# Performance work log

Hardware: AMD Instinct MI355X
Metric: run time of the kernel (lower is better)

## Reference

```python
import jax, jax.numpy as jnp
import numpy as np


def _resize_axis(x, axis, out_size):
    # PyTorch bilinear interpolate, align_corners=False, no antialias (half-pixel centers)
    in_size = x.shape[axis]
    src = (jnp.arange(out_size) + 0.5) * (in_size / out_size) - 0.5
    src = jnp.clip(src, 0.0, in_size - 1.0)
    lo = jnp.floor(src).astype(jnp.int32)
    hi = jnp.minimum(lo + 1, in_size - 1)
    w = (src - lo).astype(x.dtype)
    shp = [1] * x.ndim
    shp[axis] = out_size
    w = w.reshape(shp)
    return jnp.take(x, lo, axis=axis) * (1 - w) + jnp.take(x, hi, axis=axis) * w


def _bilinear(x, h, w):
    return _resize_axis(_resize_axis(x, 2, h), 3, w)


def _unfold3(x):
    # F.unfold(kernel_size=3, padding=1) -> [B, C, 9, H*W], kernel offsets row-major
    B, C, H, W = x.shape
    xp = jnp.pad(x, ((0, 0), (0, 0), (1, 1), (1, 1)))
    pats = jnp.stack([xp[:, :, dy:dy + H, dx:dx + W] for dy in range(3) for dx in range(3)], axis=2)
    return pats.reshape(B, C, 9, H * W)


def setup_inputs() -> dict:
    key = jax.random.key(0)
    ks = jax.random.split(key, 7)
    B, C, H, W = 4, 64, 192, 192
    return {
        "x": jax.random.normal(ks[0], (B, C, H, W), jnp.float32),
        "gn_weight": jnp.ones((C,), jnp.float32) + 0.1 * jax.random.normal(ks[1], (C,), jnp.float32),
        "gn_bias": 0.1 * jax.random.normal(ks[2], (C,), jnp.float32),
        "w1": jax.random.normal(ks[3], (2 * C, C), jnp.float32) / np.sqrt(C).astype(np.float32),
        "b1": 0.01 * jax.random.normal(ks[4], (2 * C,), jnp.float32),
        "w2": jax.random.normal(ks[5], (C, 2 * C), jnp.float32) / np.sqrt(2 * C).astype(np.float32),
        "b2": 0.01 * jax.random.normal(ks[6], (C,), jnp.float32),
    }


def reference(x, gn_weight, gn_bias, w1, b1, w2, b2):
    B, C, H, W = x.shape
    MIN_CONN, MAX_CONN, THRESHOLD, POWER = 1, 16, 0.3, 2
    KSQ = 9
    K_MAX = min(MAX_CONN, KSQ)
    EPS_NORM = 1e-12

    x_down = _bilinear(x, H // 2, W // 2)
    x_du = _bilinear(x_down, H, W)
    df = jnp.abs(x - x_du).sum(1, keepdims=True)            # [B,1,H,W]
    dmin = df.reshape(B, -1).min(1).reshape(B, 1, 1, 1)
    dmax = df.reshape(B, -1).max(1).reshape(B, 1, 1, 1)
    dfp = ((df - dmin) / (dmax - dmin + 1e-8)) ** POWER
    mask = (dfp > THRESHOLD).astype(x.dtype)
    conn = MIN_CONN + jnp.clip(jnp.round(dfp * (MAX_CONN - MIN_CONN)), 0) * mask
    counts = conn.reshape(B, H * W)                          # [B,HW]
    process = counts > 1

    # ---- per-pixel cosine similarity to 3x3 neighborhood ----
    patches = _unfold3(x)                                    # [B,C,9,HW]
    x_flat = x.reshape(B, C, H * W)
    xn = x_flat / jnp.maximum(jnp.linalg.norm(x_flat, axis=1, keepdims=True), EPS_NORM)
    pn = patches / jnp.maximum(jnp.linalg.norm(patches, axis=1, keepdims=True), EPS_NORM)
    sim = jnp.einsum('bcn,bckn->bkn', xn, pn)                # [B,9,HW]

    # ---- adaptive top-k (k = min(count, 9)) + exp-softmax weighted sum of raw patches ----
    order = jnp.argsort(-sim, axis=1)                        # descending over the 9 neighbors
    sim_s = jnp.take_along_axis(sim, order, axis=1)
    pat_s = jnp.take_along_axis(patches, jnp.broadcast_to(order[:, None], patches.shape), axis=2)
    k = jnp.minimum(counts, K_MAX)                           # [B,HW]
    keep = (jnp.arange(KSQ)[None, :, None] < k[:, None, :]).astype(x.dtype)
    wts = jnp.exp(sim_s) * keep
    wts = wts / jnp.maximum(wts.sum(1, keepdims=True), EPS_NORM)
    weighted = jnp.einsum('bckn,bkn->bcn', pat_s, wts)       # [B,C,HW]
    output = jnp.where(process[:, None, :], weighted, x_flat).reshape(B, C, H, W)

    # ---- GroupNorm(32, C) on identity ----
    G = 32
    xg = x.reshape(B, G, C // G, H, W)
    mu = xg.mean((2, 3, 4), keepdims=True)
    var = xg.var((2, 3, 4), keepdims=True)
    nx = ((xg - mu) / jnp.sqrt(var + 1e-5)).reshape(B, C, H, W)
    norm_x = nx * gn_weight[None, :, None, None] + gn_bias[None, :, None, None]

    enhanced = output + norm_x
    # ---- conv_ffn: 1x1 conv C->2C, ReLU, 1x1 conv 2C->C ----
    h1 = jax.nn.relu(jnp.einsum('oc,bchw->bohw', w1, enhanced) + b1[None, :, None, None])
    ffn = jnp.einsum('oc,bchw->bohw', w2, h1) + b2[None, :, None, None]
    return enhanced + ffn
```

## Files before the change

kernel.cpp:

```cpp
#include <hip/hip_runtime.h>
#include <hip/hip_bf16.h>

#define BB 4
#define CC 64
#define HH 192
#define WW 192
#define HWSZ (HH*WW)
#define HD 96
#define WD 96
#define GG 32
#define FTH 512
#define FPX 128
#define FBPB (HWSZ/FPX)
#define PBLK 128
#define BPB (HWSZ/PBLK)

typedef short short8 __attribute__((ext_vector_type(8)));
typedef float f32x4  __attribute__((ext_vector_type(4)));

__device__ __forceinline__ unsigned short f2bf(float f) {
    unsigned u = __float_as_uint(f);
    return (unsigned short)((u + 0x7FFFu + ((u >> 16) & 1u)) >> 16);
}
__device__ __forceinline__ float bf2f(unsigned short s) {
    return __uint_as_float(((unsigned)s) << 16);
}
__device__ __forceinline__ unsigned pk2(float a, float b) {
    return (unsigned)f2bf(a) | ((unsigned)f2bf(b) << 16);
}
__device__ __forceinline__ short8 u4s8(uint4 u) {
    union { uint4 a; short8 b; } cvt; cvt.a = u; return cvt.b;
}

__device__ __forceinline__ int swz1152(int bid) {
    return (bid & 7) * 144 + (bid >> 3);
}

__global__ __launch_bounds__(256) void k_pre(const float* __restrict__ x,
                                             const float* __restrict__ w1,
                                             const float* __restrict__ w2,
                                             unsigned* __restrict__ wf,
                                             float* __restrict__ df,
                                             float* __restrict__ nrm,
                                             float* __restrict__ gnacc,
                                             unsigned* __restrict__ mmmin,
                                             unsigned* __restrict__ mmmax) {
    __shared__ float sgn[64];
    __shared__ float wmn[4], wmx[4];
    int tid = threadIdx.x;
    if (tid < 64) sgn[tid] = 0.f;
    __syncthreads();

    if (blockIdx.x < 16) {
        #pragma unroll
        for (int rep = 0; rep < 2; ++rep) {
            int i = blockIdx.x*512 + rep*256 + tid;
            if (i < 4096) {
                float2 v = ((const float2*)w1)[i];
                int j = i >> 5, cp = i & 31, c0 = cp << 1;
                int fi = ((j >> 4) << 1) + (c0 >> 5);
                int ln = (((c0 & 31) >> 3) << 4) + (j & 15);
                wf[fi*256 + ln*4 + (cp & 3)] = pk2(v.x, v.y);
            } else {
                int i2 = i - 4096;
                float2 v = ((const float2*)w2)[i2];
                int c = i2 >> 6, jp = i2 & 63, j0 = jp << 1;
                int fi = ((j0 >> 5) << 2) + (c >> 4);
                int ln = (((j0 & 31) >> 3) << 4) + (c & 15);
                wf[4096 + fi*256 + ln*4 + (jp & 3)] = pk2(v.x, v.y);
            }
        }
    }

    int virt = swz1152(blockIdx.x);
    int b = virt / BPB;
    int pb = (virt % BPB) * PBLK;
    int wave = tid >> 6, lane = tid & 63;
    int oct = lane >> 3, grp = lane & 7;
    int p0 = pb + wave*32 + grp*4;
    int h = p0 / WW, w0 = p0 % WW;

    float hs = fminf(fmaxf(0.5f*(float)h - 0.25f, 0.f), 95.f);
    int hl = (int)hs; int hh2 = min(hl+1, 95); float fh = hs - (float)hl;
    int r0 = 2*hl, r1 = 2*hh2;

    int t0 = min(max(w0/2 - 1, 0), 92);
    float wc[4][4];
    #pragma unroll
    for (int i = 0; i < 4; ++i) {
        float wsr = fminf(fmaxf(0.5f*(float)(w0+i) - 0.25f, 0.f), 95.f);
        int wl = (int)wsr; int wh = min(wl+1, 95); float fw = wsr - (float)wl;
        int kl = wl - t0, kh = wh - t0;
        #pragma unroll
        for (int k = 0; k < 4; ++k)
            wc[i][k] = ((k==kl) ? (1.f-fw) : 0.f) + ((k==kh) ? fw : 0.f);
    }

    const float* xb = x + (size_t)b*CC*HWSZ;
    float d[4]  = {0.f,0.f,0.f,0.f};
    float qn[4] = {0.f,0.f,0.f,0.f};
    float gs[4] = {0.f,0.f,0.f,0.f};
    float gq[4] = {0.f,0.f,0.f,0.f};
    #pragma unroll
    for (int cc = 0; cc < 8; ++cc) {
        const float* pc = xb + (size_t)(oct*8 + cc)*HWSZ;
        float4 xc = *(const float4*)(pc + h*WW + w0);
        const float* pa = pc + r0*WW + 2*t0;
        const float* pq = pc + r1*WW + 2*t0;
        float T[4];
        #pragma unroll
        for (int k = 0; k < 4; ++k) {
            float2 a0 = *(const float2*)(pa + 2*k);
            float2 a1 = *(const float2*)(pa + WW + 2*k);
            float2 c0 = *(const float2*)(pq + 2*k);
            float2 c1 = *(const float2*)(pq + WW + 2*k);
            float xdA = 0.25f*((a0.x + a1.x) + (a0.y + a1.y));
            float xdB = 0.25f*((c0.x + c1.x) + (c0.y + c1.y));
            T[k] = (1.f-fh)*xdA + fh*xdB;
        }
        float xv[4] = {xc.x, xc.y, xc.z, xc.w};
        float sch = 0.f, qch = 0.f;
        #pragma unroll
        for (int i = 0; i < 4; ++i) {
            float du = (wc[i][0]*T[0] + wc[i][1]*T[1]) + (wc[i][2]*T[2] + wc[i][3]*T[3]);
            d[i] += fabsf(xv[i] - du);
            float x2 = xv[i]*xv[i];
            qn[i] += x2;
            sch += xv[i];
            qch += x2;
        }
        gs[cc>>1] += sch;
        gq[cc>>1] += qch;
    }
    #pragma unroll
    for (int o = 8; o <= 32; o <<= 1) {
        #pragma unroll
        for (int i = 0; i < 4; ++i) {
            d[i]  += __shfl_xor(d[i], o);
            qn[i] += __shfl_xor(qn[i], o);
        }
    }
    if (oct == 0) {
        *(float4*)(df  + (size_t)b*HWSZ + p0) = make_float4(d[0], d[1], d[2], d[3]);
        *(float4*)(nrm + (size_t)b*HWSZ + p0) =
            make_float4(sqrtf(qn[0]), sqrtf(qn[1]), sqrtf(qn[2]), sqrtf(qn[3]));
    }
    float mn = fminf(fminf(d[0], d[1]), fminf(d[2], d[3]));
    float mx = fmaxf(fmaxf(d[0], d[1]), fmaxf(d[2], d[3]));
    #pragma unroll
    for (int o = 1; o < 64; o <<= 1) {
        mn = fminf(mn, __shfl_xor(mn, o));
        mx = fmaxf(mx, __shfl_xor(mx, o));
    }
    if (lane == 0) { wmn[wave] = mn; wmx[wave] = mx; }
    #pragma unroll
    for (int o = 1; o <= 4; o <<= 1) {
        #pragma unroll
        for (int j = 0; j < 4; ++j) {
            gs[j] += __shfl_xor(gs[j], o);
            gq[j] += __shfl_xor(gq[j], o);
        }
    }
    if (grp == 0) {
        #pragma unroll
        for (int j = 0; j < 4; ++j) {
            atomicAdd(&sgn[2*(oct*4+j)],   gs[j]);
            atomicAdd(&sgn[2*(oct*4+j)+1], gq[j]);
        }
    }
    __syncthreads();
    if (tid < 64) atomicAdd(&gnacc[(size_t)b*64 + tid], sgn[tid]);
    if (tid == 0) {
        float bmn = fminf(fminf(wmn[0], wmn[1]), fminf(wmn[2], wmn[3]));
        float bmx = fmaxf(fmaxf(wmx[0], wmx[1]), fmaxf(wmx[2], wmx[3]));
        atomicMin(&mmmin[b], __float_as_uint(bmn));
        atomicMax(&mmmax[b], __float_as_uint(bmx));
    }
}

__global__ __launch_bounds__(FTH, 4) void k_fused(const float* __restrict__ x,
                                                  const float* __restrict__ df,
                                                  const float* __restrict__ nrm,
                                                  const unsigned* __restrict__ mmmin,
                                                  const unsigned* __restrict__ mmmax,
                                                  const float* __restrict__ gnacc,
                                                  const float* __restrict__ gw,
                                                  const float* __restrict__ gb,
                                                  const unsigned* __restrict__ wf,
                                                  const float* __restrict__ b1,
                                                  const float* __restrict__ b2,
                                                  float* __restrict__ out) {
    __shared__ __align__(16) unsigned char lds[24576];
    unsigned* se = (unsigned*)lds;
    unsigned* sh = (unsigned*)(lds + 16384);
    float* gnv = (float*)(lds + 16384);

    int tid = threadIdx.x;
    int wv = tid >> 6, lane = tid & 63;
    int q = lane >> 4, m = lane & 15;

    int virt = swz1152(blockIdx.x);
    int b = virt / FBPB;
    int pb = (virt % FBPB) * FPX;
    int pxl = wv*16 + m;
    int p = pb + pxl;
    int h = p / WW, w = p % WW;
    int cbase = q*16;

    if (tid < 32) {
        float n = 2.f*HWSZ;
        float mu  = gnacc[(size_t)b*64 + 2*tid] / n;
        float var = gnacc[(size_t)b*64 + 2*tid + 1] / n - mu*mu;
        gnv[2*tid]   = mu;
        gnv[2*tid+1] = rsqrtf(var + 1e-5f);
    }
    __syncthreads();

    float dmin = __uint_as_float(mmmin[b]);
    float dmax = __uint_as_float(mmmax[b]);
    float dfp = (df[b*HWSZ+p] - dmin) / (dmax - dmin + 1e-8f);
    dfp = dfp * dfp;
    bool maskv = dfp > 0.3f;
    float conn = 1.f + (maskv ? fmaxf(rintf(dfp * 15.f), 0.f) : 0.f);
    bool process = conn > 1.f;
    int kk = (int)fminf(conn, 9.f);

    const float* xb = x + (size_t)b*CC*HWSZ + p;
    const int dhv[9] = {-1,-1,-1, 0,0,0, 1,1,1};
    const int dwv[9] = {-1, 0, 1,-1,0,1,-1,0,1};
    bool valid[9]; int offc[9];
    #pragma unroll
    for (int j = 0; j < 9; ++j) {
        int hn = h + dhv[j], wn = w + dwv[j];
        valid[j] = (hn >= 0) && (hn < HH) && (wn >= 0) && (wn < WW);
        offc[j] = valid[j] ? (dhv[j]*WW + dwv[j]) : 0;
    }
    float wtc[9];
    #pragma unroll
    for (int j = 0; j < 9; ++j) wtc[j] = 0.f;

    if (process) {
        float dot[9];
        #pragma unroll
        for (int j = 0; j < 9; ++j) dot[j] = 0.f;
        #pragma unroll 4
        for (int cc = 0; cc < 16; ++cc) {
            const float* pc = xb + (size_t)(cbase + cc)*HWSZ;
            float xc = pc[0];
            #pragma unroll
            for (int j = 0; j < 9; ++j)
                dot[j] += xc * pc[offc[j]];
        }
        #pragma unroll
        for (int j = 0; j < 9; ++j) {
            dot[j] += __shfl_xor(dot[j], 16);
            dot[j] += __shfl_xor(dot[j], 32);
        }
        float nc = fmaxf(nrm[b*HWSZ+p], 1e-12f);
        float sim[9];
        #pragma unroll
        for (int j = 0; j < 9; ++j) {
            float nj = fmaxf(nrm[b*HWSZ+p+offc[j]], 1e-12f);
            sim[j] = valid[j] ? dot[j] / (nc * nj) : 0.f;
        }
        float S = 0.f;
        float wt[9];
        #pragma unroll
        for (int j = 0; j < 9; ++j) {
            int rank = 0;
            #pragma unroll
            for (int l = 0; l < 9; ++l)
                rank += (sim[l] > sim[j]) || (sim[l] == sim[j] && l < j);
            float ex = (rank < kk) ? expf(sim[j]) : 0.f;
            wt[j] = ex; S += ex;
        }
        float inv = 1.f / fmaxf(S, 1e-12f);
        #pragma unroll
        for (int j = 0; j < 9; ++j)
            wtc[j] = valid[j] ? wt[j] * inv : 0.f;
    }

    float e[16];
    #pragma unroll 4
    for (int cc = 0; cc < 16; ++cc) {
        int c = cbase + cc;
        const float* pc = xb + (size_t)c*HWSZ;
        float xc = pc[0];
        float oc;
        if (process) {
            float a = 0.f;
            #pragma unroll
            for (int j = 0; j < 9; ++j)
                a += wtc[j] * pc[offc[j]];
            oc = a;
        } else oc = xc;
        int g = c >> 1;
        float mu = gnv[2*g], is = gnv[2*g+1];
        e[cc] = oc + (xc - mu) * is * gw[c] + gb[c];
    }

    {
        int kc = q >> 1, qo = q & 1;
        unsigned* dst = se + (wv*2 + kc)*256;
        int la = 32*qo + m;
        uint4 ua, ub;
        ua.x = pk2(e[0],e[1]);  ua.y = pk2(e[2],e[3]);
        ua.z = pk2(e[4],e[5]);  ua.w = pk2(e[6],e[7]);
        ub.x = pk2(e[8],e[9]);  ub.y = pk2(e[10],e[11]);
        ub.z = pk2(e[12],e[13]); ub.w = pk2(e[14],e[15]);
        *(uint4*)(dst + la*4)      = ua;
        *(uint4*)(dst + (la+16)*4) = ub;
    }
    __syncthreads();

    const unsigned* wf1g = wf;
    const unsigned* wf2g = wf + 4096;
    int n16 = m;
    float b1v[8], b2v[4];
    #pragma unroll
    for (int nt = 0; nt < 8; ++nt) b1v[nt] = b1[nt*16 + n16];
    #pragma unroll
    for (int n2 = 0; n2 < 4; ++n2) b2v[n2] = b2[n2*16 + n16];

    uint4 a0 = *(uint4*)(se + (wv*2+0)*256 + lane*4);
    uint4 a1 = *(uint4*)(se + (wv*2+1)*256 + lane*4);
    f32x4 D1[8];
    #pragma unroll
    for (int nt = 0; nt < 8; ++nt) D1[nt] = (f32x4){0.f,0.f,0.f,0.f};
    #pragma unroll
    for (int nt = 0; nt < 8; ++nt) {
        uint4 bk0 = *(const uint4*)(wf1g + (nt*2+0)*256 + lane*4);
        uint4 bk1 = *(const uint4*)(wf1g + (nt*2+1)*256 + lane*4);
        D1[nt] = __builtin_amdgcn_mfma_f32_16x16x32_bf16(u4s8(a0), u4s8(bk0), D1[nt], 0, 0, 0);
        D1[nt] = __builtin_amdgcn_mfma_f32_16x16x32_bf16(u4s8(a1), u4s8(bk1), D1[nt], 0, 0, 0);
    }
    f32x4 D2[4];
    #pragma unroll
    for (int n2 = 0; n2 < 4; ++n2) D2[n2] = (f32x4){0.f,0.f,0.f,0.f};
    unsigned* shwv = sh + wv*256;
    unsigned short* shw = (unsigned short*)shwv;
    for (int kc2 = 0; kc2 < 4; ++kc2) {
        #pragma unroll
        for (int h2 = 0; h2 < 2; ++h2) {
            int nt = kc2*2 + h2;
            #pragma unroll
            for (int r = 0; r < 4; ++r) {
                float hval = fmaxf(D1[nt][r] + b1v[nt], 0.f);
                int mrow = q*4 + r;
                int k = h2*16 + n16;
                shw[((k >> 3)*16 + mrow)*8 + (k & 7)] = f2bf(hval);
            }
        }
        uint4 ah = *(uint4*)(shwv + lane*4);
        #pragma unroll
        for (int n2 = 0; n2 < 4; ++n2) {
            uint4 bb = *(const uint4*)(wf2g + (kc2*4 + n2)*256 + lane*4);
            D2[n2] = __builtin_amdgcn_mfma_f32_16x16x32_bf16(u4s8(ah), u4s8(bb), D2[n2], 0, 0, 0);
        }
    }
    float vals[4][4];
    unsigned short* seu = (unsigned short*)se;
    #pragma unroll
    for (int n2 = 0; n2 < 4; ++n2) {
        int c = n2*16 + n16;
        int kc = c >> 5, qq = (c & 31) >> 3, jj = c & 7;
        #pragma unroll
        for (int r = 0; r < 4; ++r) {
            int pxt = q*4 + r;
            float resid = bf2f(seu[((wv*2+kc)*64 + qq*16 + pxt)*8 + jj]);
            vals[n2][r] = D2[n2][r] + resid + b2v[n2];
        }
    }
    __syncthreads();

    float* stg = (float*)lds;
    float* outb = out + (size_t)b*CC*HWSZ;
    #pragma unroll
    for (int g = 0; g < 2; ++g) {
        #pragma unroll
        for (int hn2 = 0; hn2 < 2; ++hn2) {
            int n2 = 2*g + hn2;
            int row = (n2 & 1)*16 + n16;
            float4 v4 = make_float4(vals[n2][0], vals[n2][1], vals[n2][2], vals[n2][3]);
            *(float4*)&stg[row*132 + wv*16 + q*4] = v4;
        }
        __syncthreads();
        #pragma unroll
        for (int rr = 0; rr < 2; ++rr) {
            int r0 = (wv*2 + rr)*2 + (lane >> 5);
            int px4 = (lane & 31) * 4;
            float4 v = *(float4*)&stg[r0*132 + px4];
            *(float4*)&outb[(size_t)(g*32 + r0)*HWSZ + pb + px4] = v;
        }
        if (g == 0) __syncthreads();
    }
}

extern "C" void kernel_launch(void* const* d_in, const int* in_sizes, int n_in,
                              void* d_out, int out_size, void* d_ws, size_t ws_size,
                              hipStream_t stream) {
    const float* x  = (const float*)d_in[0];
    const float* gw = (const float*)d_in[1];
    const float* gb = (const float*)d_in[2];
    const float* w1 = (const float*)d_in[3];
    const float* b1 = (const float*)d_in[4];
    const float* w2 = (const float*)d_in[5];
    const float* b2 = (const float*)d_in[6];
    float* out = (float*)d_out;

    float* df       = (float*)d_ws;
    float* nrm      = df + 147456;
    float* gnacc    = nrm + 147456;
    unsigned* mmmax = (unsigned*)(gnacc + 256);
    unsigned* mmmin = mmmax + 4;
    unsigned* wf    = mmmin + 4;

    hipMemsetAsync(gnacc, 0, (256 + 4) * sizeof(float), stream);
    hipMemsetAsync(mmmin, 0xFF, 4 * sizeof(unsigned), stream);

    k_pre  <<<BB*BPB, 256, 0, stream>>>(x, w1, w2, wf, df, nrm, gnacc,
                                        mmmin, mmmax);
    k_fused<<<BB*FBPB, FTH, 0, stream>>>(x, df, nrm, mmmin, mmmax, gnacc,
                                         gw, gb, wf, b1, b2, out);
}
```

Baseline: 187.7 us.

## Write channel-last copy of x in pre-pass and read it in fused kernel

The pre-pass now also writes a transposed NHWC copy of x into workspace. The fused kernel then reads each pixel's 16 channels and its 9 neighbours with float4 loads instead of strided per-channel loads. This trades an extra full-tensor write (about 37 MB) plus its later re-read for more contiguous gathers in the similarity and aggregation loops. The path runs only when the workspace is large enough; otherwise the old path is used.

```diff
diff --git a/kernel.cpp b/kernel.cpp
--- a/kernel.cpp
+++ b/kernel.cpp
@@ -36,6 +36,7 @@
     return (bid & 7) * 144 + (bid >> 3);
 }
 
+template<int XT>
 __global__ __launch_bounds__(256) void k_pre(const float* __restrict__ x,
                                              const float* __restrict__ w1,
                                              const float* __restrict__ w2,
@@ -44,7 +45,8 @@
                                              float* __restrict__ nrm,
                                              float* __restrict__ gnacc,
                                              unsigned* __restrict__ mmmin,
-                                             unsigned* __restrict__ mmmax) {
+                                             unsigned* __restrict__ mmmax,
+                                             float* __restrict__ xt) {
     __shared__ float sgn[64];
     __shared__ float wmn[4], wmx[4];
     int tid = threadIdx.x;
@@ -102,35 +104,51 @@
     float gs[4] = {0.f,0.f,0.f,0.f};
     float gq[4] = {0.f,0.f,0.f,0.f};
     #pragma unroll
-    for (int cc = 0; cc < 8; ++cc) {
-        const float* pc = xb + (size_t)(oct*8 + cc)*HWSZ;
-        float4 xc = *(const float4*)(pc + h*WW + w0);
-        const float* pa = pc + r0*WW + 2*t0;
-        const float* pq = pc + r1*WW + 2*t0;
-        float T[4];
-        #pragma unroll
-        for (int k = 0; k < 4; ++k) {
-            float2 a0 = *(const float2*)(pa + 2*k);
-            float2 a1 = *(const float2*)(pa + WW + 2*k);
-            float2 c0 = *(const float2*)(pq + 2*k);
-            float2 c1 = *(const float2*)(pq + WW + 2*k);
-            float xdA = 0.25f*((a0.x + a1.x) + (a0.y + a1.y));
-            float xdB = 0.25f*((c0.x + c1.x) + (c0.y + c1.y));
-            T[k] = (1.f-fh)*xdA + fh*xdB;
-        }
-        float xv[4] = {xc.x, xc.y, xc.z, xc.w};
-        float sch = 0.f, qch = 0.f;
-        #pragma unroll
-        for (int i = 0; i < 4; ++i) {
-            float du = (wc[i][0]*T[0] + wc[i][1]*T[1]) + (wc[i][2]*T[2] + wc[i][3]*T[3]);
-            d[i] += fabsf(xv[i] - du);
-            float x2 = xv[i]*xv[i];
-            qn[i] += x2;
-            sch += xv[i];
-            qch += x2;
-        }
-        gs[cc>>1] += sch;
-        gq[cc>>1] += qch;
+    for (int half = 0; half < 2; ++half) {
+        float4 xbuf[4];
+        #pragma unroll
+        for (int k4 = 0; k4 < 4; ++k4) {
+            int cc = half*4 + k4;
+            const float* pc = xb + (size_t)(oct*8 + cc)*HWSZ;
+            float4 xc = *(const float4*)(pc + h*WW + w0);
+            xbuf[k4] = xc;
+            const float* pa = pc + r0*WW + 2*t0;
+            const float* pq = pc + r1*WW + 2*t0;
+            float T[4];
+            #pragma unroll
+            for (int k = 0; k < 4; ++k) {
+                float2 a0 = *(const float2*)(pa + 2*k);
+                float2 a1 = *(const float2*)(pa + WW + 2*k);
+                float2 c0 = *(const float2*)(pq + 2*k);
+                float2 c1 = *(const float2*)(pq + WW + 2*k);
+                float xdA = 0.25f*((a0.x + a1.x) + (a0.y + a1.y));
+                float xdB = 0.25f*((c0.x + c1.x) + (c0.y + c1.y));
+                T[k] = (1.f-fh)*xdA + fh*xdB;
+            }
+            float xv[4] = {xc.x, xc.y, xc.z, xc.w};
+            float sch = 0.f, qch = 0.f;
+            #pragma unroll
+            for (int i = 0; i < 4; ++i) {
+                float du = (wc[i][0]*T[0] + wc[i][1]*T[1]) + (wc[i][2]*T[2] + wc[i][3]*T[3]);
+                d[i] += fabsf(xv[i] - du);
+                float x2 = xv[i]*xv[i];
+                qn[i] += x2;
+                sch += xv[i];
+                qch += x2;
+            }
+            gs[cc>>1] += sch;
+            gq[cc>>1] += qch;
+        }
+        if (XT) {
+            #pragma unroll
+            for (int i = 0; i < 4; ++i) {
+                float4 v4 = make_float4(((const float*)&xbuf[0])[i],
+                                        ((const float*)&xbuf[1])[i],
+                                        ((const float*)&xbuf[2])[i],
+                                        ((const float*)&xbuf[3])[i]);
+                *(float4*)(xt + ((size_t)b*HWSZ + p0 + i)*CC + oct*8 + half*4) = v4;
+            }
+        }
     }
     #pragma unroll
     for (int o = 8; o <= 32; o <<= 1) {
@@ -178,7 +196,9 @@
     }
 }
 
+template<int XT>
 __global__ __launch_bounds__(FTH, 4) void k_fused(const float* __restrict__ x,
+                                                  const float* __restrict__ xt,
                                                   const float* __restrict__ df,
                                                   const float* __restrict__ nrm,
                                                   const unsigned* __restrict__ mmmin,
@@ -226,6 +246,7 @@
     int kk = (int)fminf(conn, 9.f);
 
     const float* xb = x + (size_t)b*CC*HWSZ + p;
+    const float* pt = xt + ((size_t)b*HWSZ + p)*CC + cbase;
     const int dhv[9] = {-1,-1,-1, 0,0,0, 1,1,1};
     const int dwv[9] = {-1, 0, 1,-1,0,1,-1,0,1};
     bool valid[9]; int offc[9];
@@ -243,13 +264,31 @@
         float dot[9];
         #pragma unroll
         for (int j = 0; j < 9; ++j) dot[j] = 0.f;
-        #pragma unroll 4
-        for (int cc = 0; cc < 16; ++cc) {
-            const float* pc = xb + (size_t)(cbase + cc)*HWSZ;
-            float xc = pc[0];
-            #pragma unroll
-            for (int j = 0; j < 9; ++j)
-                dot[j] += xc * pc[offc[j]];
+        if (XT) {
+            #pragma unroll
+            for (int i4 = 0; i4 < 4; ++i4) {
+                float4 X = *(const float4*)(pt + 4*i4);
+                float4 N[9];
+                #pragma unroll
+                for (int j = 0; j < 9; ++j)
+                    N[j] = *(const float4*)(pt + (ptrdiff_t)offc[j]*CC + 4*i4);
+                #pragma unroll
+                for (int r = 0; r < 4; ++r) {
+                    float xc = ((const float*)&X)[r];
+                    #pragma unroll
+                    for (int j = 0; j < 9; ++j)
+                        dot[j] += xc * ((const float*)&N[j])[r];
+                }
+            }
+        } else {
+            #pragma unroll 4
+            for (int cc = 0; cc < 16; ++cc) {
+                const float* pc = xb + (size_t)(cbase + cc)*HWSZ;
+                float xc = pc[0];
+                #pragma unroll
+                for (int j = 0; j < 9; ++j)
+                    dot[j] += xc * pc[offc[j]];
+            }
         }
         #pragma unroll
         for (int j = 0; j < 9; ++j) {
@@ -281,22 +320,52 @@
     }
 
     float e[16];
-    #pragma unroll 4
-    for (int cc = 0; cc < 16; ++cc) {
-        int c = cbase + cc;
-        const float* pc = xb + (size_t)c*HWSZ;
-        float xc = pc[0];
-        float oc;
-        if (process) {
-            float a = 0.f;
-            #pragma unroll
-            for (int j = 0; j < 9; ++j)
-                a += wtc[j] * pc[offc[j]];
-            oc = a;
-        } else oc = xc;
-        int g = c >> 1;
-        float mu = gnv[2*g], is = gnv[2*g+1];
-        e[cc] = oc + (xc - mu) * is * gw[c] + gb[c];
+    if (XT) {
+        #pragma unroll
+        for (int i4 = 0; i4 < 4; ++i4) {
+            float4 X = *(const float4*)(pt + 4*i4);
+            float4 N[9];
+            if (process) {
+                #pragma unroll
+                for (int j = 0; j < 9; ++j)
+                    N[j] = *(const float4*)(pt + (ptrdiff_t)offc[j]*CC + 4*i4);
+            }
+            #pragma unroll
+            for (int r = 0; r < 4; ++r) {
+                int cc = 4*i4 + r;
+                int c = cbase + cc;
+                float xc = ((const float*)&X)[r];
+                float oc;
+                if (process) {
+                    float a = 0.f;
+                    #pragma unroll
+                    for (int j = 0; j < 9; ++j)
+                        a += wtc[j] * ((const float*)&N[j])[r];
+                    oc = a;
+                } else oc = xc;
+                int g = c >> 1;
+                float mu = gnv[2*g], is = gnv[2*g+1];
+                e[cc] = oc + (xc - mu) * is * gw[c] + gb[c];
+            }
+        }
+    } else {
+        #pragma unroll 4
+        for (int cc = 0; cc < 16; ++cc) {
+            int c = cbase + cc;
+            const float* pc = xb + (size_t)c*HWSZ;
+            float xc = pc[0];
+            float oc;
+            if (process) {
+                float a = 0.f;
+                #pragma unroll
+                for (int j = 0; j < 9; ++j)
+                    a += wtc[j] * pc[offc[j]];
+                oc = a;
+            } else oc = xc;
+            int g = c >> 1;
+            float mu = gnv[2*g], is = gnv[2*g+1];
+            e[cc] = oc + (xc - mu) * is * gw[c] + gb[c];
+        }
     }
 
     {
@@ -414,12 +483,23 @@
     unsigned* mmmax = (unsigned*)(gnacc + 256);
     unsigned* mmmin = mmmax + 4;
     unsigned* wf    = mmmin + 4;
+    float* xtp      = (float*)(wf + 8192);
+
+    const size_t NEED = (size_t)(147456*2 + 256 + 8 + 8192 + (size_t)BB*CC*HWSZ) * 4;
+    bool big = ws_size >= NEED;
 
     hipMemsetAsync(gnacc, 0, (256 + 4) * sizeof(float), stream);
     hipMemsetAsync(mmmin, 0xFF, 4 * sizeof(unsigned), stream);
 
-    k_pre  <<<BB*BPB, 256, 0, stream>>>(x, w1, w2, wf, df, nrm, gnacc,
-                                        mmmin, mmmax);
-    k_fused<<<BB*FBPB, FTH, 0, stream>>>(x, df, nrm, mmmin, mmmax, gnacc,
-                                         gw, gb, wf, b1, b2, out);
-}
+    if (big) {
+        k_pre<1>  <<<BB*BPB, 256, 0, stream>>>(x, w1, w2, wf, df, nrm, gnacc,
+                                               mmmin, mmmax, xtp);
+        k_fused<1><<<BB*FBPB, FTH, 0, stream>>>(x, xtp, df, nrm, mmmin, mmmax,
+                                                gnacc, gw, gb, wf, b1, b2, out);
+    } else {
+        k_pre<0>  <<<BB*BPB, 256, 0, stream>>>(x, w1, w2, wf, df, nrm, gnacc,
+                                               mmmin, mmmax, nullptr);
+        k_fused<0><<<BB*FBPB, FTH, 0, stream>>>(x, nullptr, df, nrm, mmmin, mmmax,
+                                                gnacc, gw, gb, wf, b1, b2, out);
+    }
+}
```

Result: slower. 217.2 us (+15.7%).
